# Kernel optimization log

Measured on AMD Instinct MI355X. Metric: run time of the kernel, lower is better.

Reference implementation:

```python
import jax, jax.numpy as jnp
import numpy as np

C, H, W = 16, 128, 128   # in_features, dim0, dim1
FD, OUT, POOL = 3, 64, 2  # filter_dim, out_features, pooling
B = 32


def setup_inputs() -> dict:
    key = jax.random.key(0)
    k1, k2, k3 = jax.random.split(key, 3)
    x = jax.random.normal(k1, (B, C, H, W), dtype=jnp.float32)
    # linear_layer: weight (in*fd^2, out) scaled by 1/sqrt(in*fd^2), bias (out,)
    weight = jax.random.normal(k2, (C * FD * FD, OUT), dtype=jnp.float32) / jnp.sqrt(
        jnp.float32(C * FD * FD))
    bias = jax.random.normal(k3, (OUT,), dtype=jnp.float32)
    return {"x": x, "weight": weight, "bias": bias}


def reference(x, weight, bias):
    # The one-hot isometry tensordot + reshape is exactly im2col with patch
    # vector ordering c*FD^2 + n*FD + m, so the whole convolution() equals a
    # VALID conv with kernel[o, c, n, m] = weight[c*FD^2 + n*FD + m, o].
    kernel = weight.reshape(C, FD, FD, OUT).transpose(3, 0, 1, 2)  # OIHW
    y = jax.lax.conv_general_dilated(
        x, kernel, window_strides=(1, 1), padding='VALID',
        dimension_numbers=('NCHW', 'OIHW', 'NCHW'))  # (B, OUT, n_conv, m_conv)
    y = jax.nn.relu(y + bias[None, :, None, None])
    b, o, hc, wc = y.shape  # hc = H-FD+1 = 126
    # block max-pool POOLxPOOL (crop to multiple of POOL, as in the original)
    hp, wp = hc // POOL, wc // POOL
    y = y[:, :, :hp * POOL, :wp * POOL].reshape(b, o, hp, POOL, wp, POOL)
    y = jnp.max(y, axis=(3, 5))  # (B, OUT, hp, wp)
    return y.reshape(b, o, -1)  # (B, OUT, hp*wp)
```

## Files before the change

kernel.cpp:

```cpp
#include <hip/hip_runtime.h>


typedef __bf16 bf16x8 __attribute__((ext_vector_type(8)));
typedef float f32x16 __attribute__((ext_vector_type(16)));

#define MFMA32(A, B, C) __builtin_amdgcn_mfma_f32_32x32x16_bf16(A, B, C, 0, 0, 0)

__global__ void convert_b(const float* __restrict__ weight, char* __restrict__ ws) {
  int tau = blockIdx.x * 256 + threadIdx.x;
  if (tau >= 1152) return;
  int t = tau >> 7;
  int r = tau & 127;
  int o = r >> 1, hf = r & 1;
  __bf16 hi[8], lo[8];
#pragma unroll
  for (int j = 0; j < 8; ++j) {
    float v = weight[((hf * 8 + j) * 9 + t) * 64 + o];
    __bf16 h = (__bf16)v;
    hi[j] = h;
    lo[j] = (__bf16)(v - (float)h);
  }
  int nf = o >> 5, lo5 = o & 31;
  int off = (t * 2 + nf) * 1024 + (hf * 32 + lo5) * 16;
  *(bf16x8*)(ws + off) = *(bf16x8*)hi;
  *(bf16x8*)(ws + 18432 + off) = *(bf16x8*)lo;
}

__device__ __forceinline__ void stage_row(char* lds, const float* xb, int r,
                                          int colS, int hfS) {
  float v[8];
#pragma unroll
  for (int j = 0; j < 8; ++j) v[j] = xb[j * 16384 + r * 128];
  __bf16 hi[8], lo[8];
#pragma unroll
  for (int j = 0; j < 8; ++j) {
    __bf16 h = (__bf16)v[j];
    hi[j] = h;
    lo[j] = (__bf16)(v[j] - (float)h);
  }
  int a = ((r & 3) << 13) + hfS * 2048 + colS * 16;
  *(bf16x8*)(lds + a) = *(bf16x8*)hi;
  *(bf16x8*)(lds + a + 4096) = *(bf16x8*)lo;
}

__global__ __launch_bounds__(256, 2)
void convpool_main(const float* __restrict__ x, const char* __restrict__ ws,
                   const float* __restrict__ bias, float* __restrict__ out) {
  __shared__ __align__(16) char lds[48896];
  const int tid = threadIdx.x;
  const int s = blockIdx.x;
  const int b = blockIdx.y;
  const int nr = min(4, 63 - 4 * s);
  const int rb = 8 * s;
  const int lane = tid & 63;
  const int wv = tid >> 6;
  const int half = lane >> 5;
  const int lo5 = lane & 31;
  const int rr = (lane >> 4) & 1;
  const int cc = lane & 15;
  const int colS = tid >> 1;
  const int hfS = tid & 1;
  const float* xb = x + (b * 16 + hfS * 8) * 16384 + colS;

  bf16x8 Bh[9][2], Bl[9][2];
#pragma unroll
  for (int t = 0; t < 9; ++t)
#pragma unroll
    for (int nf = 0; nf < 2; ++nf) {
      int off = (t * 2 + nf) * 1024 + lane * 16;
      Bh[t][nf] = *(const bf16x8*)(ws + off);
      Bl[t][nf] = *(const bf16x8*)(ws + 18432 + off);
    }

#pragma unroll
  for (int r = 0; r < 4; ++r) stage_row(lds, xb, rb + r, colS, hfS);
  __syncthreads();

  float* ps = (float*)(lds + 32768);
  const float bv0 = bias[lo5];
  const float bv1 = bias[32 + lo5];
  const int colb16 = half * 2048 + (wv * 32 + cc) * 16;

  for (int i = 0; i < nr; ++i) {
    const int pr = 4 * s + i;
    const int i2 = 2 * i;

    f32x16 acc[2][2];
#pragma unroll
    for (int q = 0; q < 16; ++q) {
      acc[0][0][q] = 0.f; acc[0][1][q] = 0.f;
      acc[1][0][q] = 0.f; acc[1][1][q] = 0.f;
    }

#pragma unroll
    for (int t = 0; t < 9; ++t) {
      const int n = t / 3, m = t - 3 * n;
      const int sb = ((i2 + rr + n) & 3) << 13;
      const int a0 = sb + colb16 + m * 16;
      const int a1 = a0 + 256;
      bf16x8 Ah0 = *(const bf16x8*)(lds + a0);
      bf16x8 Ah1 = *(const bf16x8*)(lds + a1);
      bf16x8 Al0 = *(const bf16x8*)(lds + a0 + 4096);
      bf16x8 Al1 = *(const bf16x8*)(lds + a1 + 4096);
      acc[0][0] = MFMA32(Ah0, Bh[t][0], acc[0][0]);
      acc[1][0] = MFMA32(Ah1, Bh[t][0], acc[1][0]);
      acc[0][1] = MFMA32(Ah0, Bh[t][1], acc[0][1]);
      acc[1][1] = MFMA32(Ah1, Bh[t][1], acc[1][1]);
      acc[0][0] = MFMA32(Al0, Bh[t][0], acc[0][0]);
      acc[1][0] = MFMA32(Al1, Bh[t][0], acc[1][0]);
      acc[0][1] = MFMA32(Al0, Bh[t][1], acc[0][1]);
      acc[1][1] = MFMA32(Al1, Bh[t][1], acc[1][1]);
      acc[0][0] = MFMA32(Ah0, Bl[t][0], acc[0][0]);
      acc[1][0] = MFMA32(Ah1, Bl[t][0], acc[1][0]);
      acc[0][1] = MFMA32(Ah0, Bl[t][1], acc[0][1]);
      acc[1][1] = MFMA32(Ah1, Bl[t][1], acc[1][1]);
    }

#pragma unroll
    for (int mt = 0; mt < 2; ++mt)
#pragma unroll
      for (int nf = 0; nf < 2; ++nf) {
        const f32x16 a = acc[mt][nf];
        const int o = nf * 32 + lo5;
        const float bvv = nf ? bv1 : bv0;
#pragma unroll
        for (int g = 0; g < 4; ++g) {
          float mx = fmaxf(fmaxf(a[2 * g], a[2 * g + 1]),
                           fmaxf(a[8 + 2 * g], a[9 + 2 * g]));
          float v = fmaxf(mx + bvv, 0.0f);
          int pcc = 2 * half + (g & 1) + 4 * (g >> 1);
          int pc = (wv * 2 + mt) * 8 + pcc;
          if (pc < 63) ps[o * 63 + pc] = v;
        }
      }
    __syncthreads();

    if (i < nr - 1) {
      stage_row(lds, xb, rb + i2 + 4, colS, hfS);
      stage_row(lds, xb, rb + i2 + 5, colS, hfS);
    }
    {
      const int ob = ((b * 64) * 63 + pr) * 63;
#pragma unroll
      for (int v = 0; v < 16; ++v) {
        int idx = tid + 256 * v;
        if (idx < 4032) {
          int o = idx / 63;
          int pc = idx - o * 63;
          out[ob + o * 3969 + pc] = ps[idx];
        }
      }
    }
    __syncthreads();
  }
}

extern "C" void kernel_launch(void* const* d_in, const int* in_sizes, int n_in,
                              void* d_out, int out_size, void* d_ws, size_t ws_size,
                              hipStream_t stream) {
  const float* x = (const float*)d_in[0];
  const float* wgt = (const float*)d_in[1];
  const float* bias = (const float*)d_in[2];
  float* out = (float*)d_out;
  char* ws = (char*)d_ws;
  convert_b<<<dim3(5), 256, 0, stream>>>(wgt, ws);
  convpool_main<<<dim3(16, 32), 256, 0, stream>>>(x, ws, bias, out);
}
```

Before: 37.99 us.

## Halve rows per block, prefetch next rows into registers, raise occupancy

Each block now produces two pooled rows instead of four, and the grid doubles to 32x32 so more blocks run in parallel. The global loads for the next two input rows are issued into registers before the MFMA compute of the current row, and are written to LDS after it, so load latency overlaps with compute. The kernel also raises MFMA wave priority during the compute loop and asks for 3 blocks per CU. In exchange, the initial four-row staging is amortised over fewer output rows and register pressure rises from the prefetch buffers.

New measurement: 75.92 us. 2x slower.

```diff
diff --git a/kernel.cpp b/kernel.cpp
--- a/kernel.cpp
+++ b/kernel.cpp
@@ -26,11 +26,8 @@
   *(bf16x8*)(ws + 18432 + off) = *(bf16x8*)lo;
 }
 
-__device__ __forceinline__ void stage_row(char* lds, const float* xb, int r,
-                                          int colS, int hfS) {
-  float v[8];
-#pragma unroll
-  for (int j = 0; j < 8; ++j) v[j] = xb[j * 16384 + r * 128];
+__device__ __forceinline__ void write_staged(char* lds, const float* v, int r,
+                                             int colS, int hfS) {
   __bf16 hi[8], lo[8];
 #pragma unroll
   for (int j = 0; j < 8; ++j) {
@@ -43,15 +40,90 @@
   *(bf16x8*)(lds + a + 4096) = *(bf16x8*)lo;
 }
 
-__global__ __launch_bounds__(256, 2)
+__device__ __forceinline__ void load_row(const float* xb, int r, float* v) {
+#pragma unroll
+  for (int j = 0; j < 8; ++j) v[j] = xb[j * 16384 + r * 128];
+}
+
+__device__ __forceinline__ void compute_row(const char* lds, float* ps,
+                                            const bf16x8 Bh[9][2],
+                                            const bf16x8 Bl[9][2], int i2,
+                                            int colb16, int rr, int half,
+                                            int lo5, int wv, float bv0,
+                                            float bv1) {
+  f32x16 acc[2][2];
+#pragma unroll
+  for (int q = 0; q < 16; ++q) {
+    acc[0][0][q] = 0.f; acc[0][1][q] = 0.f;
+    acc[1][0][q] = 0.f; acc[1][1][q] = 0.f;
+  }
+  __builtin_amdgcn_s_setprio(1);
+#pragma unroll
+  for (int t = 0; t < 9; ++t) {
+    const int n = t / 3, m = t - 3 * n;
+    const int sb = ((i2 + rr + n) & 3) << 13;
+    const int a0 = sb + colb16 + m * 16;
+    const int a1 = a0 + 256;
+    bf16x8 Ah0 = *(const bf16x8*)(lds + a0);
+    bf16x8 Ah1 = *(const bf16x8*)(lds + a1);
+    bf16x8 Al0 = *(const bf16x8*)(lds + a0 + 4096);
+    bf16x8 Al1 = *(const bf16x8*)(lds + a1 + 4096);
+    acc[0][0] = MFMA32(Ah0, Bh[t][0], acc[0][0]);
+    acc[1][0] = MFMA32(Ah1, Bh[t][0], acc[1][0]);
+    acc[0][1] = MFMA32(Ah0, Bh[t][1], acc[0][1]);
+    acc[1][1] = MFMA32(Ah1, Bh[t][1], acc[1][1]);
+    acc[0][0] = MFMA32(Al0, Bh[t][0], acc[0][0]);
+    acc[1][0] = MFMA32(Al1, Bh[t][0], acc[1][0]);
+    acc[0][1] = MFMA32(Al0, Bh[t][1], acc[0][1]);
+    acc[1][1] = MFMA32(Al1, Bh[t][1], acc[1][1]);
+    acc[0][0] = MFMA32(Ah0, Bl[t][0], acc[0][0]);
+    acc[1][0] = MFMA32(Ah1, Bl[t][0], acc[1][0]);
+    acc[0][1] = MFMA32(Ah0, Bl[t][1], acc[0][1]);
+    acc[1][1] = MFMA32(Ah1, Bl[t][1], acc[1][1]);
+  }
+  __builtin_amdgcn_s_setprio(0);
+#pragma unroll
+  for (int mt = 0; mt < 2; ++mt)
+#pragma unroll
+    for (int nf = 0; nf < 2; ++nf) {
+      const f32x16 a = acc[mt][nf];
+      const int o = nf * 32 + lo5;
+      const float bvv = nf ? bv1 : bv0;
+#pragma unroll
+      for (int g = 0; g < 4; ++g) {
+        float mx = fmaxf(fmaxf(a[2 * g], a[2 * g + 1]),
+                         fmaxf(a[8 + 2 * g], a[9 + 2 * g]));
+        float v = fmaxf(mx + bvv, 0.0f);
+        int pcc = 2 * half + (g & 1) + 4 * (g >> 1);
+        int pc = (wv * 2 + mt) * 8 + pcc;
+        if (pc < 63) ps[o * 63 + pc] = v;
+      }
+    }
+}
+
+__device__ __forceinline__ void store_out(const float* ps, float* out, int b,
+                                          int pr, int tid) {
+  const int ob = ((b * 64) * 63 + pr) * 63;
+#pragma unroll
+  for (int v = 0; v < 16; ++v) {
+    int idx = tid + 256 * v;
+    if (idx < 4032) {
+      int o = idx / 63;
+      int pc = idx - o * 63;
+      out[ob + o * 3969 + pc] = ps[idx];
+    }
+  }
+}
+
+__global__ __launch_bounds__(256, 3)
 void convpool_main(const float* __restrict__ x, const char* __restrict__ ws,
                    const float* __restrict__ bias, float* __restrict__ out) {
   __shared__ __align__(16) char lds[48896];
   const int tid = threadIdx.x;
   const int s = blockIdx.x;
   const int b = blockIdx.y;
-  const int nr = min(4, 63 - 4 * s);
-  const int rb = 8 * s;
+  const int rb = 4 * s;
+  const bool two = (s < 31);
   const int lane = tid & 63;
   const int wv = tid >> 6;
   const int half = lane >> 5;
@@ -73,7 +145,11 @@
     }
 
 #pragma unroll
-  for (int r = 0; r < 4; ++r) stage_row(lds, xb, rb + r, colS, hfS);
+  for (int r = 0; r < 4; ++r) {
+    float v[8];
+    load_row(xb, rb + r, v);
+    write_staged(lds, v, rb + r, colS, hfS);
+  }
   __syncthreads();
 
   float* ps = (float*)(lds + 32768);
@@ -81,77 +157,24 @@
   const float bv1 = bias[32 + lo5];
   const int colb16 = half * 2048 + (wv * 32 + cc) * 16;
 
-  for (int i = 0; i < nr; ++i) {
-    const int pr = 4 * s + i;
-    const int i2 = 2 * i;
+  float v0[8], v1[8];
+  if (two) {
+    load_row(xb, rb + 4, v0);
+    load_row(xb, rb + 5, v1);
+  }
+  compute_row(lds, ps, Bh, Bl, 0, colb16, rr, half, lo5, wv, bv0, bv1);
+  __syncthreads();
+  if (two) {
+    write_staged(lds, v0, rb + 4, colS, hfS);
+    write_staged(lds, v1, rb + 5, colS, hfS);
+  }
+  store_out(ps, out, b, 2 * s, tid);
 
-    f32x16 acc[2][2];
-#pragma unroll
-    for (int q = 0; q < 16; ++q) {
-      acc[0][0][q] = 0.f; acc[0][1][q] = 0.f;
-      acc[1][0][q] = 0.f; acc[1][1][q] = 0.f;
-    }
-
-#pragma unroll
-    for (int t = 0; t < 9; ++t) {
-      const int n = t / 3, m = t - 3 * n;
-      const int sb = ((i2 + rr + n) & 3) << 13;
-      const int a0 = sb + colb16 + m * 16;
-      const int a1 = a0 + 256;
-      bf16x8 Ah0 = *(const bf16x8*)(lds + a0);
-      bf16x8 Ah1 = *(const bf16x8*)(lds + a1);
-      bf16x8 Al0 = *(const bf16x8*)(lds + a0 + 4096);
-      bf16x8 Al1 = *(const bf16x8*)(lds + a1 + 4096);
-      acc[0][0] = MFMA32(Ah0, Bh[t][0], acc[0][0]);
-      acc[1][0] = MFMA32(Ah1, Bh[t][0], acc[1][0]);
-      acc[0][1] = MFMA32(Ah0, Bh[t][1], acc[0][1]);
-      acc[1][1] = MFMA32(Ah1, Bh[t][1], acc[1][1]);
-      acc[0][0] = MFMA32(Al0, Bh[t][0], acc[0][0]);
-      acc[1][0] = MFMA32(Al1, Bh[t][0], acc[1][0]);
-      acc[0][1] = MFMA32(Al0, Bh[t][1], acc[0][1]);
-      acc[1][1] = MFMA32(Al1, Bh[t][1], acc[1][1]);
-      acc[0][0] = MFMA32(Ah0, Bl[t][0], acc[0][0]);
-      acc[1][0] = MFMA32(Ah1, Bl[t][0], acc[1][0]);
-      acc[0][1] = MFMA32(Ah0, Bl[t][1], acc[0][1]);
-      acc[1][1] = MFMA32(Ah1, Bl[t][1], acc[1][1]);
-    }
-
-#pragma unroll
-    for (int mt = 0; mt < 2; ++mt)
-#pragma unroll
-      for (int nf = 0; nf < 2; ++nf) {
-        const f32x16 a = acc[mt][nf];
-        const int o = nf * 32 + lo5;
-        const float bvv = nf ? bv1 : bv0;
-#pragma unroll
-        for (int g = 0; g < 4; ++g) {
-          float mx = fmaxf(fmaxf(a[2 * g], a[2 * g + 1]),
-                           fmaxf(a[8 + 2 * g], a[9 + 2 * g]));
-          float v = fmaxf(mx + bvv, 0.0f);
-          int pcc = 2 * half + (g & 1) + 4 * (g >> 1);
-          int pc = (wv * 2 + mt) * 8 + pcc;
-          if (pc < 63) ps[o * 63 + pc] = v;
-        }
-      }
+  if (two) {
     __syncthreads();
-
-    if (i < nr - 1) {
-      stage_row(lds, xb, rb + i2 + 4, colS, hfS);
-      stage_row(lds, xb, rb + i2 + 5, colS, hfS);
-    }
-    {
-      const int ob = ((b * 64) * 63 + pr) * 63;
-#pragma unroll
-      for (int v = 0; v < 16; ++v) {
-        int idx = tid + 256 * v;
-        if (idx < 4032) {
-          int o = idx / 63;
-          int pc = idx - o * 63;
-          out[ob + o * 3969 + pc] = ps[idx];
-        }
-      }
-    }
+    compute_row(lds, ps, Bh, Bl, 2, colb16, rr, half, lo5, wv, bv0, bv1);
     __syncthreads();
+    store_out(ps, out, b, 2 * s + 1, tid);
   }
 }
 
@@ -164,5 +187,5 @@
   float* out = (float*)d_out;
   char* ws = (char*)d_ws;
   convert_b<<<dim3(5), 256, 0, stream>>>(wgt, ws);
-  convpool_main<<<dim3(16, 32), 256, 0, stream>>>(x, ws, bias, out);
+  convpool_main<<<dim3(32, 32), 256, 0, stream>>>(x, ws, bias, out);
 }
```
